# Performance work log

Measured on AMD Instinct MI355X. Metric: run time of the kernel, lower is better.

Reference implementation:

```python
import jax, jax.numpy as jnp
from jax import lax
import numpy as np

EPS = 1e-5


def conv2d(x, w, b, stride, pad):
    y = lax.conv_general_dilated(x, w, (stride, stride), [(pad, pad), (pad, pad)],
                                 dimension_numbers=('NCHW', 'OIHW', 'NCHW'))
    return y + b[None, :, None, None]


def conv_transpose2d(x, w, b, stride, pad, opad):
    # w in torch ConvTranspose2d layout: (Cin, Cout, kH, kW)
    k = w.shape[2]
    w_f = jnp.flip(w, (2, 3)).transpose(1, 0, 2, 3)  # -> OIHW
    lo = k - 1 - pad
    y = lax.conv_general_dilated(x, w_f, (1, 1), [(lo, lo + opad), (lo, lo + opad)],
                                 lhs_dilation=(stride, stride),
                                 dimension_numbers=('NCHW', 'OIHW', 'NCHW'))
    return y + b[None, :, None, None]


def batchnorm(x, g, b):
    # training-mode BN: batch statistics over (N, H, W)
    mean = jnp.mean(x, axis=(0, 2, 3), keepdims=True)
    var = jnp.var(x, axis=(0, 2, 3), keepdims=True)
    return (x - mean) * lax.rsqrt(var + EPS) * g[None, :, None, None] + b[None, :, None, None]


def quantize(z, codebook):
    # z: (B, C, H, W), codebook: (K, C)
    B, C, H, W = z.shape
    zf = z.transpose(0, 2, 3, 1).reshape(-1, C)  # (B*H*W, C)
    # squared Euclidean distances (argmin-equivalent to torch.cdist p=2)
    d2 = (jnp.sum(zf * zf, axis=1, keepdims=True)
          - 2.0 * zf @ codebook.T
          + jnp.sum(codebook * codebook, axis=1)[None, :])
    idx = jnp.argmin(d2, axis=-1)                # (B*H*W,)
    quant = codebook[idx]                        # gather
    loss_embed = jnp.mean((lax.stop_gradient(zf) - quant) ** 2)
    loss_commit = jnp.mean((zf - lax.stop_gradient(quant)) ** 2)
    quant_out = zf + lax.stop_gradient(quant - zf)  # straight-through
    quant_out = quant_out.reshape(B, H, W, C).transpose(0, 3, 1, 2)
    return quant_out, loss_embed, loss_commit, idx.reshape(B, H * W)


def setup_inputs() -> dict:
    key = jax.random.key(0)
    ks = jax.random.split(key, 20)
    f32 = jnp.float32

    def w(k, shape):
        fan_in = int(np.prod(shape[1:]))
        return jax.random.normal(k, shape, f32) / np.sqrt(fan_in)

    B, IMG = 64, 128
    C0, C1, C2, LAT, K = 3, 128, 256, 64, 512
    return {
        'x': jax.random.normal(ks[0], (B, C0, IMG, IMG), f32),
        'enc1_w': w(ks[1], (C1, C0, 3, 3)), 'enc1_b': jnp.zeros((C1,), f32),
        'bn1_g': jnp.ones((C1,), f32), 'bn1_b': jnp.zeros((C1,), f32),
        'enc2_w': w(ks[2], (C2, C1, 3, 3)), 'enc2_b': jnp.zeros((C2,), f32),
        'pre_w': w(ks[3], (LAT, C2, 1, 1)), 'pre_b': jnp.zeros((LAT,), f32),
        'codebook': jax.random.normal(ks[4], (K, LAT), f32),
        'post_w': w(ks[5], (C2, LAT, 1, 1)), 'post_b': jnp.zeros((C2,), f32),
        'dec1_w': w(ks[6], (C2, C1, 3, 3)), 'dec1_b': jnp.zeros((C1,), f32),
        'dbn1_g': jnp.ones((C1,), f32), 'dbn1_b': jnp.zeros((C1,), f32),
        'dec2_w': w(ks[7], (C1, C0, 3, 3)), 'dec2_b': jnp.zeros((C0,), f32),
    }


def reference(x, enc1_w, enc1_b, bn1_g, bn1_b, enc2_w, enc2_b, pre_w, pre_b,
              codebook, post_w, post_b, dec1_w, dec1_b, dbn1_g, dbn1_b,
              dec2_w, dec2_b):
    # encoder
    h = jax.nn.relu(batchnorm(conv2d(x, enc1_w, enc1_b, 2, 1), bn1_g, bn1_b))
    h = conv2d(h, enc2_w, enc2_b, 2, 1)          # (B, 256, 32, 32), no BN/act on last enc conv
    z = conv2d(h, pre_w, pre_b, 1, 0)            # (B, 64, 32, 32)
    # VQ codebook lookup
    q, loss_embed, loss_commit, idx = quantize(z, codebook)
    # decoder
    d = conv2d(q, post_w, post_b, 1, 0)          # (B, 256, 32, 32)
    d = jax.nn.relu(batchnorm(conv_transpose2d(d, dec1_w, dec1_b, 2, 1, 1), dbn1_g, dbn1_b))
    recon = jnp.tanh(conv_transpose2d(d, dec2_w, dec2_b, 2, 1, 1))  # (B, 3, 128, 128)
    return recon, loss_embed, loss_commit, idx
```

## Files before the change

### kernel.cpp

```cpp
#include <hip/hip_runtime.h>

#define EPS 1e-5f

typedef __attribute__((ext_vector_type(8))) short short8;
typedef __attribute__((ext_vector_type(4))) float f32x4;
typedef _Float16 half8v __attribute__((ext_vector_type(8)));

__device__ inline ushort f2bf(float f) {
    uint u = __float_as_uint(f);
    u += 0x7FFFu + ((u >> 16) & 1u);
    return (ushort)(u >> 16);
}
__device__ inline float bf2f(ushort h) { return __uint_as_float(((uint)h) << 16); }
__device__ inline ushort hbits(_Float16 h) { return __builtin_bit_cast(ushort, h); }

#define WS_BN1SUM   0
#define WS_LOSS     512
#define WS_BN1SC    1024
#define WS_BN1SH    1152
#define WS_BN2SC    1280
#define WS_BN2SH    1408
#define WS_CC       1536
#define WS_IDX      2048
#define WS_WT3      67584
#define WS_WT1      83968
#define WS_WT2      378880
#define WS_F        673792
#define WS_BN2S8    804864
#define WS_BN1S8    806912
#define WS_WTE1     808960
#define WS_A        1048576
#define WS_B        34603008
#define WS_Z        WS_A

#define OUT_LOSS_E  3145728
#define OUT_LOSS_C  3145729
#define OUT_IDX     3145730

__global__ __launch_bounds__(256) void k_wt(const float* __restrict__ dec1_w,
                                            const float* __restrict__ enc2_w,
                                            const float* __restrict__ pre_w,
                                            const float* __restrict__ enc1_w,
                                            float* __restrict__ ws) {
    int g = blockIdx.x * 256 + threadIdx.x;
    if (g < 294912) {
        int ci = g & 255, co = (g >> 8) & 127, tap = g >> 15;
        float v = dec1_w[ci * 1152 + co * 9 + tap];
        ushort hi = f2bf(v);
        ushort lo = f2bf(v - bf2f(hi));
        ushort* u16 = (ushort*)(ws + WS_WT1);
        u16[g] = hi;
        u16[294912 + g] = lo;
    } else if (g < 2 * 294912) {
        int h = g - 294912;
        int ci = h & 127, rest = h >> 7;
        int co = rest & 255, tap = rest >> 8;
        float v = enc2_w[co * 1152 + ci * 9 + tap];
        _Float16 hi = (_Float16)v;
        _Float16 lo = (_Float16)((v - (float)hi) * 2048.0f);
        ushort* u16 = (ushort*)(ws + WS_WT2);
        u16[h] = hbits(hi);
        u16[294912 + h] = hbits(lo);
    } else if (g < 2 * 294912 + 16384) {
        int h = g - 2 * 294912;
        int co = h & 63, ci = h >> 6;
        ws[WS_WT3 + h] = pre_w[co * 256 + ci];
    } else if (g < 2 * 294912 + 16384 + 4096) {
        int h = g - (2 * 294912 + 16384);
        int k = h & 31, co = h >> 5;
        float v = (k < 27) ? enc1_w[co * 27 + k] : 0.f;
        _Float16 hi = (_Float16)v;
        _Float16 lo = (_Float16)((v - (float)hi) * 2048.0f);
        ushort* u16 = (ushort*)(ws + WS_WTE1);
        u16[h] = hbits(hi);
        u16[4096 + h] = hbits(lo);
    }
}

__global__ __launch_bounds__(256) void k_F(const float* __restrict__ codebook,
                                           const float* __restrict__ post_w,
                                           const float* __restrict__ post_b,
                                           float* __restrict__ ws) {
    __shared__ __align__(16) float cbr[64];
    int k = blockIdx.x, co = threadIdx.x;
    if (co < 64) cbr[co] = codebook[k * 64 + co];
    __syncthreads();
    float acc = post_b[co];
#pragma unroll
    for (int i = 0; i < 64; i += 4) {
        float4 w4 = *(const float4*)&post_w[co * 64 + i];
        acc = fmaf(cbr[i], w4.x, acc);
        acc = fmaf(cbr[i + 1], w4.y, acc);
        acc = fmaf(cbr[i + 2], w4.z, acc);
        acc = fmaf(cbr[i + 3], w4.w, acc);
    }
    ws[WS_F + k * 256 + co] = acc;
    if (co == 0) {
        float s = 0.f;
        for (int i = 0; i < 64; i++) s += cbr[i] * cbr[i];
        ws[WS_CC + k] = s;
    }
}

__global__ __launch_bounds__(256, 2) void k_enc1(const float* __restrict__ x,
                                                 const float* __restrict__ bias,
                                                 float* __restrict__ ws) {
    __shared__ __align__(16) float raw_s[1950];
    __shared__ __align__(16) ushort As_h[5120], As_l[5120];
    int b = blockIdx.x;
    int n = b >> 5, oy0 = (b & 31) * 2;
    int tid = threadIdx.x, lane = tid & 63, wid = tid >> 6;
    int wy = wid >> 1, wx = wid & 1;
    int l15 = lane & 15, quad = lane >> 4;
    int co0 = wx * 64;
    const ushort* we1h = (const ushort*)(ws + WS_WTE1);
    const ushort* we1l = we1h + 4096;

    half8v Bh[4], Bl[4];
#pragma unroll
    for (int nt = 0; nt < 4; nt++) {
        int src = (co0 + nt * 16 + l15) * 32 + quad * 8;
        Bh[nt] = *(const half8v*)&we1h[src];
        Bl[nt] = *(const half8v*)&we1l[src];
    }

    for (int i = tid; i < 1950; i += 256) {
        int c = i % 130, rest = i / 130;
        int rr = rest % 5, ci = rest / 5;
        int iy = 2 * oy0 - 1 + rr, ix = c - 1;
        float v = 0.f;
        if ((unsigned)iy < 128u && (unsigned)ix < 128u)
            v = x[(n * 3 + ci) * 16384 + iy * 128 + ix];
        raw_s[i] = v;
    }
    __syncthreads();

    for (int i = tid; i < 4096; i += 256) {
        int m = i >> 5, k = i & 31;
        float v = 0.f;
        if (k < 27) {
            int ci = k / 9, t9 = k - ci * 9;
            int ky = t9 / 3, kx = t9 - ky * 3;
            int r = m >> 6, xx = m & 63;
            v = raw_s[(ci * 5 + 2 * r + ky) * 130 + 2 * xx + kx];
        }
        _Float16 hi = (_Float16)v;
        _Float16 lo = (_Float16)((v - (float)hi) * 2048.f);
        As_h[m * 40 + k] = hbits(hi);
        As_l[m * 40 + k] = hbits(lo);
    }
    __syncthreads();

    f32x4 acc1[4][4], acc2[4][4];
#pragma unroll
    for (int nt = 0; nt < 4; nt++) {
        float bv = bias[co0 + nt * 16 + l15];
#pragma unroll
        for (int mt = 0; mt < 4; mt++) {
            acc1[mt][nt] = (f32x4){bv, bv, bv, bv};
            acc2[mt][nt] = (f32x4){0.f, 0.f, 0.f, 0.f};
        }
    }

    half8v Ah[4], Al[4];
#pragma unroll
    for (int mt = 0; mt < 4; mt++) {
        int aoff = (wy * 64 + mt * 16 + l15) * 40 + quad * 8;
        Ah[mt] = *(const half8v*)&As_h[aoff];
        Al[mt] = *(const half8v*)&As_l[aoff];
    }
#pragma unroll
    for (int nt = 0; nt < 4; nt++)
#pragma unroll
        for (int mt = 0; mt < 4; mt++) {
            acc2[mt][nt] = __builtin_amdgcn_mfma_f32_16x16x32_f16(Ah[mt], Bl[nt], acc2[mt][nt], 0, 0, 0);
            acc2[mt][nt] = __builtin_amdgcn_mfma_f32_16x16x32_f16(Al[mt], Bh[nt], acc2[mt][nt], 0, 0, 0);
            acc1[mt][nt] = __builtin_amdgcn_mfma_f32_16x16x32_f16(Ah[mt], Bh[nt], acc1[mt][nt], 0, 0, 0);
        }

    float* h1 = ws + WS_A;
    const float ls = 1.f / 2048.f;
    int oy = oy0 + wy;
#pragma unroll
    for (int mt = 0; mt < 4; mt++) {
        int x0 = mt * 16 + quad * 4;
#pragma unroll
        for (int nt = 0; nt < 4; nt++) {
            int co = co0 + nt * 16 + l15;
            *(float4*)&h1[((n * 128 + co) * 64 + oy) * 64 + x0] =
                make_float4(fmaf(acc2[mt][nt][0], ls, acc1[mt][nt][0]),
                            fmaf(acc2[mt][nt][1], ls, acc1[mt][nt][1]),
                            fmaf(acc2[mt][nt][2], ls, acc1[mt][nt][2]),
                            fmaf(acc2[mt][nt][3], ls, acc1[mt][nt][3]));
        }
    }
    int shadow = (b & 7) * 256;
#pragma unroll
    for (int nt = 0; nt < 4; nt++) {
        float s1 = 0.f, s2 = 0.f;
#pragma unroll
        for (int mt = 0; mt < 4; mt++)
#pragma unroll
            for (int r = 0; r < 4; r++) {
                float v = fmaf(acc2[mt][nt][r], ls, acc1[mt][nt][r]);
                s1 += v; s2 += v * v;
            }
        s1 += __shfl_xor(s1, 16); s1 += __shfl_xor(s1, 32);
        s2 += __shfl_xor(s2, 16); s2 += __shfl_xor(s2, 32);
        if (quad == 0) {
            int co = co0 + nt * 16 + l15;
            atomicAdd(&ws[WS_BN1S8 + shadow + co], s1);
            atomicAdd(&ws[WS_BN1S8 + shadow + 128 + co], s2);
        }
    }
}

__global__ __launch_bounds__(128) void k_bnfin8(const float* __restrict__ sums8,
                                                const float* __restrict__ g,
                                                const float* __restrict__ b,
                                                float* __restrict__ scale,
                                                float* __restrict__ shift) {
    int c = threadIdx.x;
    float s1 = 0.f, s2 = 0.f;
    for (int k = 0; k < 8; k++) {
        s1 += sums8[k * 256 + c];
        s2 += sums8[k * 256 + 128 + c];
    }
    float mean = s1 * (1.f / 262144.f);
    float var = s2 * (1.f / 262144.f) - mean * mean;
    float sc = g[c] * rsqrtf(var + EPS);
    scale[c] = sc;
    shift[c] = b[c] - mean * sc;
}

__global__ __launch_bounds__(256, 2) void k_enc2(const float* __restrict__ bias,
                                                 float* __restrict__ ws) {
    __shared__ __align__(16) uint As_h[6500], As_l[6500];
    __shared__ float scs[128], shs[128];
    int b = blockIdx.x;
    int n = b >> 4, y0 = (b & 15) * 2;
    int tid = threadIdx.x, lane = tid & 63, wid = tid >> 6;
    int l15 = lane & 15, quad = lane >> 4;
    int co0 = wid * 64;
    const float* h1 = ws + WS_A;
    const ushort* w2h = (const ushort*)(ws + WS_WT2);
    const ushort* w2l = w2h + 294912;

    if (tid < 128) { scs[tid] = ws[WS_BN1SC + tid]; shs[tid] = ws[WS_BN1SH + tid]; }

    int Abase[4];
#pragma unroll
    for (int mt = 0; mt < 4; mt++) {
        int m = mt * 16 + l15;
        Abase[mt] = (2 * (m >> 5)) * 2600 + (2 * (m & 31)) * 40 + quad * 8;
    }

    f32x4 acc1[4][4], acc2[4][4];
#pragma unroll
    for (int nt = 0; nt < 4; nt++) {
        float bv = bias[co0 + nt * 16 + l15];
#pragma unroll
        for (int mt = 0; mt < 4; mt++) {
            acc1[mt][nt] = (f32x4){bv, bv, bv, bv};
            acc2[mt][nt] = (f32x4){0.f, 0.f, 0.f, 0.f};
        }
    }

    for (int c0 = 0; c0 < 128; c0 += 32) {
        __syncthreads();
        if (tid < 80) {
            int p = tid & 15, row = tid >> 4;
            As_h[row * 1300 + p] = 0;
            As_l[row * 1300 + p] = 0;
        }
        for (int i = tid; i < 1280; i += 256) {
            int p = i & 15, g = i >> 4;
            int row = g >> 4, colg = g & 15;
            int in_y = 2 * y0 - 1 + row;
            int ci0 = c0 + 2 * p;
            float av[4] = {0.f, 0.f, 0.f, 0.f}, bv[4] = {0.f, 0.f, 0.f, 0.f};
            if ((unsigned)in_y < 64u) {
                const float* bp = h1 + (n * 128 + ci0) * 4096 + in_y * 64 + colg * 4;
                float4 va = *(const float4*)bp;
                float4 vb = *(const float4*)(bp + 4096);
                float sa = scs[ci0], ta = shs[ci0];
                float sb = scs[ci0 + 1], tb = shs[ci0 + 1];
                av[0] = fmaxf(fmaf(va.x, sa, ta), 0.f); av[1] = fmaxf(fmaf(va.y, sa, ta), 0.f);
                av[2] = fmaxf(fmaf(va.z, sa, ta), 0.f); av[3] = fmaxf(fmaf(va.w, sa, ta), 0.f);
                bv[0] = fmaxf(fmaf(vb.x, sb, tb), 0.f); bv[1] = fmaxf(fmaf(vb.y, sb, tb), 0.f);
                bv[2] = fmaxf(fmaf(vb.z, sb, tb), 0.f); bv[3] = fmaxf(fmaf(vb.w, sb, tb), 0.f);
            }
            int wbase = row * 1300 + (colg * 4 + 1) * 20 + p;
#pragma unroll
            for (int j = 0; j < 4; j++) {
                _Float16 ah = (_Float16)av[j], bh = (_Float16)bv[j];
                _Float16 al = (_Float16)((av[j] - (float)ah) * 2048.f);
                _Float16 bl = (_Float16)((bv[j] - (float)bh) * 2048.f);
                As_h[wbase + j * 20] = (uint)hbits(ah) | ((uint)hbits(bh) << 16);
                As_l[wbase + j * 20] = (uint)hbits(al) | ((uint)hbits(bl) << 16);
            }
        }
        __syncthreads();
        const ushort* ah16 = (const ushort*)As_h;
        const ushort* al16 = (const ushort*)As_l;
#pragma unroll
        for (int tap = 0; tap < 9; tap++) {
            int ky = tap / 3, kx = tap - ky * 3;
            int toff = ky * 2600 + kx * 40;
            half8v Bh[4], Bl[4];
#pragma unroll
            for (int nt = 0; nt < 4; nt++) {
                int src = (tap * 256 + co0 + nt * 16 + l15) * 128 + c0 + quad * 8;
                Bh[nt] = *(const half8v*)&w2h[src];
                Bl[nt] = *(const half8v*)&w2l[src];
            }
            half8v Ah[4], Al[4];
#pragma unroll
            for (int mt = 0; mt < 4; mt++) {
                Ah[mt] = *(const half8v*)&ah16[Abase[mt] + toff];
                Al[mt] = *(const half8v*)&al16[Abase[mt] + toff];
            }
#pragma unroll
            for (int nt = 0; nt < 4; nt++)
#pragma unroll
                for (int mt = 0; mt < 4; mt++) {
                    acc2[mt][nt] = __builtin_amdgcn_mfma_f32_16x16x32_f16(Ah[mt], Bl[nt], acc2[mt][nt], 0, 0, 0);
                    acc2[mt][nt] = __builtin_amdgcn_mfma_f32_16x16x32_f16(Al[mt], Bh[nt], acc2[mt][nt], 0, 0, 0);
                    acc1[mt][nt] = __builtin_amdgcn_mfma_f32_16x16x32_f16(Ah[mt], Bh[nt], acc1[mt][nt], 0, 0, 0);
                }
        }
    }

    float* h2 = ws + WS_B;
    const float ls = 1.f / 2048.f;
#pragma unroll
    for (int mt = 0; mt < 4; mt++) {
        int mloc = mt * 16 + quad * 4;
        int y = y0 + (mloc >> 5), x = mloc & 31;
#pragma unroll
        for (int nt = 0; nt < 4; nt++) {
            int co = co0 + nt * 16 + l15;
            *(float4*)&h2[(n * 256 + co) * 1024 + y * 32 + x] =
                make_float4(fmaf(acc2[mt][nt][0], ls, acc1[mt][nt][0]),
                            fmaf(acc2[mt][nt][1], ls, acc1[mt][nt][1]),
                            fmaf(acc2[mt][nt][2], ls, acc1[mt][nt][2]),
                            fmaf(acc2[mt][nt][3], ls, acc1[mt][nt][3]));
        }
    }
}

__global__ __launch_bounds__(256) void k_pre(const float* __restrict__ bias,
                                             float* __restrict__ ws) {
    __shared__ __align__(16) float a_s[8 * 128];
    __shared__ __align__(16) float b_s[8 * 64];
    int p0 = blockIdx.x * 128;
    int n = p0 >> 10, sp0 = p0 & 1023;
    int tid = threadIdx.x;
    int px4 = tid & 31, cg = tid >> 5;
    int co8 = cg * 8;
    const float* h2 = ws + WS_B;
    const float* wt3 = ws + WS_WT3;

    float acc[4][8];
#pragma unroll
    for (int r = 0; r < 4; r++)
#pragma unroll
        for (int j = 0; j < 8; j++) acc[r][j] = bias[co8 + j];

    for (int c0 = 0; c0 < 256; c0 += 8) {
        __syncthreads();
#pragma unroll
        for (int it = 0; it < 4; it++) {
            int t = tid + it * 256;
            a_s[t] = h2[n * 262144 + (c0 + (t >> 7)) * 1024 + sp0 + (t & 127)];
        }
#pragma unroll
        for (int it = 0; it < 2; it++) {
            int t = tid + it * 256;
            b_s[t] = wt3[(c0 + (t >> 6)) * 64 + (t & 63)];
        }
        __syncthreads();
#pragma unroll
        for (int ci = 0; ci < 8; ci++) {
            float4 av = *(const float4*)&a_s[ci * 128 + px4 * 4];
            float4 w0 = *(const float4*)&b_s[ci * 64 + co8];
            float4 w1 = *(const float4*)&b_s[ci * 64 + co8 + 4];
            float wv[8] = {w0.x, w0.y, w0.z, w0.w, w1.x, w1.y, w1.z, w1.w};
            float a[4] = {av.x, av.y, av.z, av.w};
#pragma unroll
            for (int j = 0; j < 8; j++)
#pragma unroll
                for (int r = 0; r < 4; r++) acc[r][j] = fmaf(a[r], wv[j], acc[r][j]);
        }
    }
    float* z = ws + WS_Z;
#pragma unroll
    for (int r = 0; r < 4; r++) {
        int p = p0 + px4 * 4 + r;
        *(float4*)&z[p * 64 + co8] = make_float4(acc[r][0], acc[r][1], acc[r][2], acc[r][3]);
        *(float4*)&z[p * 64 + co8 + 4] = make_float4(acc[r][4], acc[r][5], acc[r][6], acc[r][7]);
    }
}

__global__ __launch_bounds__(256, 2) void k_vq(const float* __restrict__ codebook,
                                               float* __restrict__ out,
                                               float* __restrict__ ws) {
    __shared__ __align__(16) float cb_s[128 * 64];
    __shared__ __align__(16) float cc_s[128];
    int tid = threadIdx.x;
    int p = blockIdx.x * 256 + tid;
    const float* z = ws + WS_Z + p * 64;
    float4 z4[16];
#pragma unroll
    for (int i = 0; i < 16; i++) z4[i] = *(const float4*)&z[i * 4];
    float zz = 0.f;
#pragma unroll
    for (int i = 0; i < 16; i++)
        zz += z4[i].x * z4[i].x + z4[i].y * z4[i].y + z4[i].z * z4[i].z + z4[i].w * z4[i].w;

    float best = 3.4e38f;
    int bidx = 0;
    for (int k0 = 0; k0 < 512; k0 += 128) {
        __syncthreads();
#pragma unroll
        for (int it = 0; it < 32; it++) {
            int t = tid + it * 256;
            cb_s[t] = codebook[k0 * 64 + t];
        }
        if (tid < 128) cc_s[tid] = ws[WS_CC + k0 + tid];
        __syncthreads();
        for (int k = 0; k < 128; k++) {
            const float4* cp = (const float4*)&cb_s[k * 64];
            float d0 = 0.f, d1 = 0.f, d2 = 0.f, d3 = 0.f;
#pragma unroll
            for (int i = 0; i < 16; i += 4) {
                float4 c0v = cp[i], c1v = cp[i + 1], c2v = cp[i + 2], c3v = cp[i + 3];
                d0 += z4[i].x * c0v.x + z4[i].y * c0v.y + z4[i].z * c0v.z + z4[i].w * c0v.w;
                d1 += z4[i + 1].x * c1v.x + z4[i + 1].y * c1v.y + z4[i + 1].z * c1v.z + z4[i + 1].w * c1v.w;
                d2 += z4[i + 2].x * c2v.x + z4[i + 2].y * c2v.y + z4[i + 2].z * c2v.z + z4[i + 2].w * c2v.w;
                d3 += z4[i + 3].x * c3v.x + z4[i + 3].y * c3v.y + z4[i + 3].z * c3v.z + z4[i + 3].w * c3v.w;
            }
            float dot = (d0 + d1) + (d2 + d3);
            float d = fmaf(-2.f, dot, zz) + cc_s[k];
            if (d < best) { best = d; bidx = k0 + k; }
        }
    }
    out[OUT_IDX + p] = (float)bidx;
    ((int*)(ws + WS_IDX))[p] = bidx;

    float e = 0.f;
    const float4* q = (const float4*)&codebook[bidx * 64];
#pragma unroll
    for (int i = 0; i < 16; i++) {
        float4 qq = q[i];
        float d0 = z4[i].x - qq.x, d1 = z4[i].y - qq.y;
        float d2 = z4[i].z - qq.z, d3 = z4[i].w - qq.w;
        e += d0 * d0 + d1 * d1 + d2 * d2 + d3 * d3;
    }
#pragma unroll
    for (int off = 32; off; off >>= 1) e += __shfl_down(e, off);
    if ((tid & 63) == 0) atomicAdd(&ws[WS_LOSS], e);
}

__global__ void k_loss(float* __restrict__ out, const float* __restrict__ ws) {
    if (threadIdx.x == 0) {
        float v = ws[WS_LOSS] * (1.f / (65536.f * 64.f));
        out[OUT_LOSS_E] = v;
        out[OUT_LOSS_C] = v;
    }
}

__global__ __launch_bounds__(256) void k_gather(float* __restrict__ ws) {
    int tid = threadIdx.x;
    const int* idx = (const int*)(ws + WS_IDX);
    const float* F = ws + WS_F;
    float* dpx = ws + WS_B;
    int base = blockIdx.x * 64;
    for (int i = 0; i < 64; i++) {
        int row = idx[base + i];
        dpx[(base + i) * 256 + tid] = F[row * 256 + tid];
    }
}

__global__ __launch_bounds__(256, 2) void k_dec1(const float* __restrict__ bias,
                                                 float* __restrict__ ws) {
    __shared__ __align__(16) short As_h[5280], As_l[5280];
    __shared__ __align__(16) short Bs_h[4096], Bs_l[4096];
    int bx = blockIdx.x;
    int tile = bx & 511, phase = bx >> 9;
    int py = phase >> 1, px = phase & 1;
    int n_img = tile >> 3, a0 = (tile & 7) * 4;
    int tid = threadIdx.x, lane = tid & 63, wid = tid >> 6;
    int wy = wid >> 1, wx = wid & 1;
    int l15 = lane & 15, quad = lane >> 4;

    int ntY = py + 1, ntX = px + 1, ntap = ntY * ntX;
    int tap_off[4], tap_w[4];
    {
        int ti = 0;
        for (int ty = 0; ty < ntY; ty++)
            for (int tx = 0; tx < ntX; tx++) {
                int dy = py ? 1 - ty : 0, ky = py ? 2 * ty : 1;
                int dx = px ? 1 - tx : 0, kx = px ? 2 * tx : 1;
                tap_off[ti] = (dy * 33 + dx) * 32;
                tap_w[ti] = ky * 3 + kx;
                ti++;
            }
    }

    int Aoff[4];
#pragma unroll
    for (int mt = 0; mt < 4; mt++) {
        int m_loc = wy * 64 + mt * 16 + l15;
        Aoff[mt] = ((m_loc >> 5) * 33 + (m_loc & 31)) * 32 + quad * 8;
    }
    int Boff[4];
#pragma unroll
    for (int nt = 0; nt < 4; nt++)
        Boff[nt] = (wx * 64 + nt * 16 + l15) * 32 + quad * 8;

    f32x4 acc[4][4];
#pragma unroll
    for (int nt = 0; nt < 4; nt++) {
        float bv = bias[wx * 64 + nt * 16 + l15];
#pragma unroll
        for (int mt = 0; mt < 4; mt++) acc[mt][nt] = (f32x4){bv, bv, bv, bv};
    }

    const float* dpx = ws + WS_B;
    const ushort* wbh = (const ushort*)(ws + WS_WT1);
    const ushort* wbl = wbh + 294912;

    for (int c0 = 0; c0 < 256; c0 += 32) {
        __syncthreads();
        for (int i = tid; i < 1320; i += 256) {
            int p5 = i >> 3, q = i & 7;
            int rr = p5 / 33, cc = p5 - rr * 33;
            int a_in = a0 + rr;
            float4 v = make_float4(0.f, 0.f, 0.f, 0.f);
            if (a_in < 32 && cc < 32)
                v = *(const float4*)&dpx[(n_img * 1024 + a_in * 32 + cc) * 256 + c0 + q * 4];
            ushort h0 = f2bf(v.x), h1 = f2bf(v.y), h2 = f2bf(v.z), h3v = f2bf(v.w);
            ushort l0 = f2bf(v.x - bf2f(h0)), l1 = f2bf(v.y - bf2f(h1));
            ushort l2 = f2bf(v.z - bf2f(h2)), l3 = f2bf(v.w - bf2f(h3v));
            int d = p5 * 32 + q * 4;
            *(uint*)&As_h[d]     = (uint)h0 | ((uint)h1 << 16);
            *(uint*)&As_h[d + 2] = (uint)h2 | ((uint)h3v << 16);
            *(uint*)&As_l[d]     = (uint)l0 | ((uint)l1 << 16);
            *(uint*)&As_l[d + 2] = (uint)l2 | ((uint)l3 << 16);
        }
        for (int t = 0; t < ntap; t++) {
            if (t) __syncthreads();
            int tw = tap_w[t];
            for (int i = tid; i < 512; i += 256) {
                int co = i >> 2, q = i & 3;
                int src = (tw * 128 + co) * 256 + c0 + q * 8;
                *(uint4*)&Bs_h[co * 32 + q * 8] = *(const uint4*)&wbh[src];
                *(uint4*)&Bs_l[co * 32 + q * 8] = *(const uint4*)&wbl[src];
            }
            __syncthreads();
            int ao = tap_off[t];
            short8 Ah[4], Al[4];
#pragma unroll
            for (int mt = 0; mt < 4; mt++) {
                Ah[mt] = *(const short8*)&As_h[Aoff[mt] + ao];
                Al[mt] = *(const short8*)&As_l[Aoff[mt] + ao];
            }
#pragma unroll
            for (int nt = 0; nt < 4; nt++) {
                short8 Bh = *(const short8*)&Bs_h[Boff[nt]];
                short8 Bl = *(const short8*)&Bs_l[Boff[nt]];
#pragma unroll
                for (int mt = 0; mt < 4; mt++) {
                    acc[mt][nt] = __builtin_amdgcn_mfma_f32_16x16x32_bf16(Ah[mt], Bh, acc[mt][nt], 0, 0, 0);
                    acc[mt][nt] = __builtin_amdgcn_mfma_f32_16x16x32_bf16(Ah[mt], Bl, acc[mt][nt], 0, 0, 0);
                    acc[mt][nt] = __builtin_amdgcn_mfma_f32_16x16x32_bf16(Al[mt], Bh, acc[mt][nt], 0, 0, 0);
                }
            }
        }
    }

    float* h3n = ws + WS_A;
#pragma unroll
    for (int mt = 0; mt < 4; mt++) {
#pragma unroll
        for (int r = 0; r < 4; r++) {
            int m_glob = tile * 128 + wy * 64 + mt * 16 + quad * 4 + r;
            int a = (m_glob >> 5) & 31, bb = m_glob & 31;
            int y = 2 * a + py, x = 2 * bb + px;
            float* rowp = &h3n[(((m_glob >> 10) * 64 + y) * 64 + x) * 128 + wx * 64];
#pragma unroll
            for (int nt = 0; nt < 4; nt++) rowp[nt * 16 + l15] = acc[mt][nt][r];
        }
    }
    int shadow = (bx & 7) * 256;
#pragma unroll
    for (int nt = 0; nt < 4; nt++) {
        float s1 = 0.f, s2 = 0.f;
#pragma unroll
        for (int mt = 0; mt < 4; mt++)
#pragma unroll
            for (int r = 0; r < 4; r++) {
                float v = acc[mt][nt][r];
                s1 += v; s2 += v * v;
            }
        s1 += __shfl_xor(s1, 16); s1 += __shfl_xor(s1, 32);
        s2 += __shfl_xor(s2, 16); s2 += __shfl_xor(s2, 32);
        if (quad == 0) {
            int co = wx * 64 + nt * 16 + l15;
            atomicAdd(&ws[WS_BN2S8 + shadow + co], s1);
            atomicAdd(&ws[WS_BN2S8 + shadow + 128 + co], s2);
        }
    }
}

__global__ __launch_bounds__(1024, 2) void k_dec2(const float* __restrict__ w,
                                                  const float* __restrict__ bias,
                                                  float* __restrict__ out,
                                                  float* __restrict__ ws) {
    __shared__ __align__(16) float in_s[8 * 5 * 66];
    __shared__ __align__(16) float w_s[8 * 9 * 3];
    __shared__ float scs[128], shs[128];
    int n = blockIdx.y;
    int atile = blockIdx.x;
    int a0 = atile * 4;
    int tid = threadIdx.x;
    int phase = tid >> 8;
    int py = phase >> 1, px = phase & 1;
    int tidl = tid & 255;
    int b = tidl & 63, r4 = tidl >> 6;
    int ntsh = py + px;
    int ntap = 1 << ntsh;
    const float* h3n = ws + WS_A;

    if (tid < 128) { scs[tid] = ws[WS_BN2SC + tid]; shs[tid] = ws[WS_BN2SH + tid]; }

    float acc[3] = {bias[0], bias[1], bias[2]};
    for (int c0 = 0; c0 < 128; c0 += 8) {
        __syncthreads();
        if (tid < 660) {
            int ciq = tid & 1, s = tid >> 1;
            int cL = s % 66, row = s / 66;
            int iy = a0 + row;
            float r0 = 0.f, r1 = 0.f, r2 = 0.f, r3 = 0.f;
            if (iy < 64 && cL < 64) {
                float4 v = *(const float4*)&h3n[((n * 64 + iy) * 64 + cL) * 128 + c0 + ciq * 4];
                int cb = c0 + ciq * 4;
                r0 = fmaxf(fmaf(v.x, scs[cb], shs[cb]), 0.f);
                r1 = fmaxf(fmaf(v.y, scs[cb + 1], shs[cb + 1]), 0.f);
                r2 = fmaxf(fmaf(v.z, scs[cb + 2], shs[cb + 2]), 0.f);
                r3 = fmaxf(fmaf(v.w, scs[cb + 3], shs[cb + 3]), 0.f);
            }
            int ci0 = ciq * 4;
            in_s[(ci0 + 0) * 330 + row * 66 + cL] = r0;
            in_s[(ci0 + 1) * 330 + row * 66 + cL] = r1;
            in_s[(ci0 + 2) * 330 + row * 66 + cL] = r2;
            in_s[(ci0 + 3) * 330 + row * 66 + cL] = r3;
        }
        if (tid < 8 * 9 * 3) {
            int co = tid % 3, q = tid / 3;
            int ci = q / 9, tap = q - ci * 9;
            w_s[q * 3 + co] = w[(c0 + ci) * 27 + co * 9 + tap];
        }
        __syncthreads();
#pragma unroll
        for (int ci = 0; ci < 8; ci++) {
#pragma unroll
            for (int tt = 0; tt < 4; tt++) {
                if (tt >= ntap) break;
                int ty = tt >> px, tx = tt & px;
                int ky = py ? 2 * ty : 1;
                int kx = px ? 2 * tx : 1;
                int dyv = py ? 1 - ty : 0;
                int dxv = px ? 1 - tx : 0;
                float v = in_s[ci * 330 + (r4 + dyv) * 66 + b + dxv];
                const float* wp = &w_s[(ci * 9 + ky * 3 + kx) * 3];
                acc[0] = fmaf(v, wp[0], acc[0]);
                acc[1] = fmaf(v, wp[1], acc[1]);
                acc[2] = fmaf(v, wp[2], acc[2]);
            }
        }
    }
    int y = 2 * (a0 + r4) + py, xcol = 2 * b + px;
#pragma unroll
    for (int co = 0; co < 3; co++)
        out[(n * 3 + co) * 16384 + y * 128 + xcol] = tanhf(acc[co]);
}

extern "C" void kernel_launch(void* const* d_in, const int* in_sizes, int n_in,
                              void* d_out, int out_size, void* d_ws, size_t ws_size,
                              hipStream_t stream) {
    const float* x       = (const float*)d_in[0];
    const float* enc1_w  = (const float*)d_in[1];
    const float* enc1_b  = (const float*)d_in[2];
    const float* bn1_g   = (const float*)d_in[3];
    const float* bn1_b   = (const float*)d_in[4];
    const float* enc2_w  = (const float*)d_in[5];
    const float* enc2_b  = (const float*)d_in[6];
    const float* pre_w   = (const float*)d_in[7];
    const float* pre_b   = (const float*)d_in[8];
    const float* codebook= (const float*)d_in[9];
    const float* post_w  = (const float*)d_in[10];
    const float* post_b  = (const float*)d_in[11];
    const float* dec1_w  = (const float*)d_in[12];
    const float* dec1_b  = (const float*)d_in[13];
    const float* dbn1_g  = (const float*)d_in[14];
    const float* dbn1_b  = (const float*)d_in[15];
    const float* dec2_w  = (const float*)d_in[16];
    const float* dec2_b  = (const float*)d_in[17];
    float* out = (float*)d_out;
    float* ws  = (float*)d_ws;

    hipMemsetAsync(ws, 0, 4096, stream);
    hipMemsetAsync(ws + WS_BN2S8, 0, 2 * 8 * 256 * 4, stream);

    k_wt<<<2384, 256, 0, stream>>>(dec1_w, enc2_w, pre_w, enc1_w, ws);
    k_F<<<512, 256, 0, stream>>>(codebook, post_w, post_b, ws);
    k_enc1<<<2048, 256, 0, stream>>>(x, enc1_b, ws);
    k_bnfin8<<<1, 128, 0, stream>>>(ws + WS_BN1S8, bn1_g, bn1_b,
                                    ws + WS_BN1SC, ws + WS_BN1SH);
    k_enc2<<<1024, 256, 0, stream>>>(enc2_b, ws);
    k_pre<<<512, 256, 0, stream>>>(pre_b, ws);
    k_vq<<<256, 256, 0, stream>>>(codebook, out, ws);
    k_loss<<<1, 64, 0, stream>>>(out, ws);
    k_gather<<<1024, 256, 0, stream>>>(ws);
    k_dec1<<<2048, 256, 0, stream>>>(dec1_b, ws);
    k_bnfin8<<<1, 128, 0, stream>>>(ws + WS_BN2S8, dbn1_g, dbn1_b,
                                    ws + WS_BN2SC, ws + WS_BN2SH);
    k_dec2<<<dim3(16, 64), 1024, 0, stream>>>(dec2_w, dec2_b, out, ws);
}
```

Baseline: 856.7 us.

## Compute VQ distances with split-fp16 MFMA and derive loss from min distance

The scalar FP32 codebook-distance loop in k_vq becomes split-fp16 (hi/lo) MFMA matrix multiplies. Each block handles 64 pixels and each wave scans 128 codes, then an argmin is reduced across lanes and waves with ties broken toward the lower index. The codebook is pre-split into fp16 hi/lo in k_wt. The loss is now taken as zz plus the minimum distance rather than recomputed against the gathered code. This can cause small rounding differences and argmin flips on near-ties, and the loss can pick up cancellation error.

```diff
diff --git a/kernel.cpp b/kernel.cpp
--- a/kernel.cpp
+++ b/kernel.cpp
@@ -14,7 +14,6 @@
 __device__ inline float bf2f(ushort h) { return __uint_as_float(((uint)h) << 16); }
 __device__ inline ushort hbits(_Float16 h) { return __builtin_bit_cast(ushort, h); }
 
-#define WS_BN1SUM   0
 #define WS_LOSS     512
 #define WS_BN1SC    1024
 #define WS_BN1SH    1152
@@ -29,6 +28,7 @@
 #define WS_BN2S8    804864
 #define WS_BN1S8    806912
 #define WS_WTE1     808960
+#define WS_CBS      819200
 #define WS_A        1048576
 #define WS_B        34603008
 #define WS_Z        WS_A
@@ -41,6 +41,7 @@
                                             const float* __restrict__ enc2_w,
                                             const float* __restrict__ pre_w,
                                             const float* __restrict__ enc1_w,
+                                            const float* __restrict__ codebook,
                                             float* __restrict__ ws) {
     int g = blockIdx.x * 256 + threadIdx.x;
     if (g < 294912) {
@@ -74,6 +75,14 @@
         ushort* u16 = (ushort*)(ws + WS_WTE1);
         u16[h] = hbits(hi);
         u16[4096 + h] = hbits(lo);
+    } else if (g < 2 * 294912 + 16384 + 4096 + 32768) {
+        int h = g - (2 * 294912 + 16384 + 4096);
+        float v = codebook[h];
+        _Float16 hi = (_Float16)v;
+        _Float16 lo = (_Float16)((v - (float)hi) * 2048.0f);
+        ushort* u16 = (ushort*)(ws + WS_CBS);
+        u16[h] = hbits(hi);
+        u16[32768 + h] = hbits(lo);
     }
 }
 
@@ -402,64 +411,137 @@
     }
 }
 
-__global__ __launch_bounds__(256, 2) void k_vq(const float* __restrict__ codebook,
-                                               float* __restrict__ out,
+__global__ __launch_bounds__(256, 2) void k_vq(float* __restrict__ out,
                                                float* __restrict__ ws) {
-    __shared__ __align__(16) float cb_s[128 * 64];
-    __shared__ __align__(16) float cc_s[128];
-    int tid = threadIdx.x;
-    int p = blockIdx.x * 256 + tid;
-    const float* z = ws + WS_Z + p * 64;
-    float4 z4[16];
-#pragma unroll
-    for (int i = 0; i < 16; i++) z4[i] = *(const float4*)&z[i * 4];
-    float zz = 0.f;
-#pragma unroll
-    for (int i = 0; i < 16; i++)
-        zz += z4[i].x * z4[i].x + z4[i].y * z4[i].y + z4[i].z * z4[i].z + z4[i].w * z4[i].w;
-
-    float best = 3.4e38f;
-    int bidx = 0;
-    for (int k0 = 0; k0 < 512; k0 += 128) {
-        __syncthreads();
-#pragma unroll
-        for (int it = 0; it < 32; it++) {
-            int t = tid + it * 256;
-            cb_s[t] = codebook[k0 * 64 + t];
-        }
-        if (tid < 128) cc_s[tid] = ws[WS_CC + k0 + tid];
-        __syncthreads();
-        for (int k = 0; k < 128; k++) {
-            const float4* cp = (const float4*)&cb_s[k * 64];
-            float d0 = 0.f, d1 = 0.f, d2 = 0.f, d3 = 0.f;
-#pragma unroll
-            for (int i = 0; i < 16; i += 4) {
-                float4 c0v = cp[i], c1v = cp[i + 1], c2v = cp[i + 2], c3v = cp[i + 3];
-                d0 += z4[i].x * c0v.x + z4[i].y * c0v.y + z4[i].z * c0v.z + z4[i].w * c0v.w;
-                d1 += z4[i + 1].x * c1v.x + z4[i + 1].y * c1v.y + z4[i + 1].z * c1v.z + z4[i + 1].w * c1v.w;
-                d2 += z4[i + 2].x * c2v.x + z4[i + 2].y * c2v.y + z4[i + 2].z * c2v.z + z4[i + 2].w * c2v.w;
-                d3 += z4[i + 3].x * c3v.x + z4[i + 3].y * c3v.y + z4[i + 3].z * c3v.z + z4[i + 3].w * c3v.w;
-            }
-            float dot = (d0 + d1) + (d2 + d3);
-            float d = fmaf(-2.f, dot, zz) + cc_s[k];
-            if (d < best) { best = d; bidx = k0 + k; }
-        }
-    }
-    out[OUT_IDX + p] = (float)bidx;
-    ((int*)(ws + WS_IDX))[p] = bidx;
-
-    float e = 0.f;
-    const float4* q = (const float4*)&codebook[bidx * 64];
-#pragma unroll
-    for (int i = 0; i < 16; i++) {
-        float4 qq = q[i];
-        float d0 = z4[i].x - qq.x, d1 = z4[i].y - qq.y;
-        float d2 = z4[i].z - qq.z, d3 = z4[i].w - qq.w;
-        e += d0 * d0 + d1 * d1 + d2 * d2 + d3 * d3;
-    }
-#pragma unroll
-    for (int off = 32; off; off >>= 1) e += __shfl_down(e, off);
-    if ((tid & 63) == 0) atomicAdd(&ws[WS_LOSS], e);
+    __shared__ __align__(16) ushort Ash[64 * 72], Asl[64 * 72];
+    __shared__ float zz_s[64];
+    __shared__ float red_s[256];
+    __shared__ int red_i[256];
+    int p0 = blockIdx.x * 64;
+    int tid = threadIdx.x, lane = tid & 63, wid = tid >> 6;
+    int l15 = lane & 15, quad = lane >> 4;
+    const float* z = ws + WS_Z;
+    const ushort* cbh = (const ushort*)(ws + WS_CBS);
+    const ushort* cbl = cbh + 32768;
+
+    for (int i = tid; i < 1024; i += 256) {
+        int m = i >> 4, k4 = (i & 15) * 4;
+        float4 v = *(const float4*)&z[(p0 + m) * 64 + k4];
+        _Float16 h0 = (_Float16)v.x, h1 = (_Float16)v.y, h2 = (_Float16)v.z, h3 = (_Float16)v.w;
+        _Float16 l0 = (_Float16)((v.x - (float)h0) * 2048.f);
+        _Float16 l1 = (_Float16)((v.y - (float)h1) * 2048.f);
+        _Float16 l2 = (_Float16)((v.z - (float)h2) * 2048.f);
+        _Float16 l3 = (_Float16)((v.w - (float)h3) * 2048.f);
+        int d = m * 72 + k4;
+        *(uint*)&Ash[d]     = (uint)hbits(h0) | ((uint)hbits(h1) << 16);
+        *(uint*)&Ash[d + 2] = (uint)hbits(h2) | ((uint)hbits(h3) << 16);
+        *(uint*)&Asl[d]     = (uint)hbits(l0) | ((uint)hbits(l1) << 16);
+        *(uint*)&Asl[d + 2] = (uint)hbits(l2) | ((uint)hbits(l3) << 16);
+    }
+    if (tid < 64) {
+        const float* zp = &z[(p0 + tid) * 64];
+        float s = 0.f;
+#pragma unroll
+        for (int k = 0; k < 64; k += 4) {
+            float4 v = *(const float4*)&zp[k];
+            s += v.x * v.x + v.y * v.y + v.z * v.z + v.w * v.w;
+        }
+        zz_s[tid] = s;
+    }
+    __syncthreads();
+
+    float best_s[4][4];
+    int best_i[4][4];
+#pragma unroll
+    for (int mt = 0; mt < 4; mt++)
+#pragma unroll
+        for (int r = 0; r < 4; r++) { best_s[mt][r] = 3.4e38f; best_i[mt][r] = 0; }
+
+    const float ls = 1.f / 2048.f;
+    for (int pass = 0; pass < 2; pass++) {
+        f32x4 acc1[4][4], acc2[4][4];
+#pragma unroll
+        for (int mt = 0; mt < 4; mt++)
+#pragma unroll
+            for (int nt = 0; nt < 4; nt++) {
+                acc1[mt][nt] = (f32x4){0.f, 0.f, 0.f, 0.f};
+                acc2[mt][nt] = (f32x4){0.f, 0.f, 0.f, 0.f};
+            }
+#pragma unroll
+        for (int kc = 0; kc < 2; kc++) {
+            half8v Ah[4], Al[4];
+#pragma unroll
+            for (int mt = 0; mt < 4; mt++) {
+                int aoff = (mt * 16 + l15) * 72 + kc * 32 + quad * 8;
+                Ah[mt] = *(const half8v*)&Ash[aoff];
+                Al[mt] = *(const half8v*)&Asl[aoff];
+            }
+#pragma unroll
+            for (int nt = 0; nt < 4; nt++) {
+                int code = wid * 128 + pass * 64 + nt * 16 + l15;
+                int src = code * 64 + kc * 32 + quad * 8;
+                half8v Bh = *(const half8v*)&cbh[src];
+                half8v Bl = *(const half8v*)&cbl[src];
+#pragma unroll
+                for (int mt = 0; mt < 4; mt++) {
+                    acc2[mt][nt] = __builtin_amdgcn_mfma_f32_16x16x32_f16(Ah[mt], Bl, acc2[mt][nt], 0, 0, 0);
+                    acc2[mt][nt] = __builtin_amdgcn_mfma_f32_16x16x32_f16(Al[mt], Bh, acc2[mt][nt], 0, 0, 0);
+                    acc1[mt][nt] = __builtin_amdgcn_mfma_f32_16x16x32_f16(Ah[mt], Bh, acc1[mt][nt], 0, 0, 0);
+                }
+            }
+        }
+#pragma unroll
+        for (int nt = 0; nt < 4; nt++) {
+            int code = wid * 128 + pass * 64 + nt * 16 + l15;
+            float cc = ws[WS_CC + code];
+#pragma unroll
+            for (int mt = 0; mt < 4; mt++)
+#pragma unroll
+                for (int r = 0; r < 4; r++) {
+                    float dot = fmaf(acc2[mt][nt][r], ls, acc1[mt][nt][r]);
+                    float s = fmaf(-2.f, dot, cc);
+                    if (s < best_s[mt][r] || (s == best_s[mt][r] && code < best_i[mt][r])) {
+                        best_s[mt][r] = s; best_i[mt][r] = code;
+                    }
+                }
+        }
+    }
+
+#pragma unroll
+    for (int mt = 0; mt < 4; mt++)
+#pragma unroll
+        for (int r = 0; r < 4; r++) {
+            float s = best_s[mt][r];
+            int ix = best_i[mt][r];
+#pragma unroll
+            for (int off = 1; off < 16; off <<= 1) {
+                float so = __shfl_xor(s, off);
+                int io = __shfl_xor(ix, off);
+                if (so < s || (so == s && io < ix)) { s = so; ix = io; }
+            }
+            if (l15 == 0) {
+                int px = mt * 16 + quad * 4 + r;
+                red_s[wid * 64 + px] = s;
+                red_i[wid * 64 + px] = ix;
+            }
+        }
+    __syncthreads();
+    if (tid < 64) {
+        float s = red_s[tid];
+        int ix = red_i[tid];
+#pragma unroll
+        for (int w = 1; w < 4; w++) {
+            float so = red_s[w * 64 + tid];
+            int io = red_i[w * 64 + tid];
+            if (so < s || (so == s && io < ix)) { s = so; ix = io; }
+        }
+        out[OUT_IDX + p0 + tid] = (float)ix;
+        ((int*)(ws + WS_IDX))[p0 + tid] = ix;
+        float e = fmaxf(zz_s[tid] + s, 0.f);
+#pragma unroll
+        for (int off = 32; off; off >>= 1) e += __shfl_down(e, off);
+        if (tid == 0) atomicAdd(&ws[WS_LOSS], e);
+    }
 }
 
 __global__ void k_loss(float* __restrict__ out, const float* __restrict__ ws) {
@@ -714,14 +796,14 @@
     hipMemsetAsync(ws, 0, 4096, stream);
     hipMemsetAsync(ws + WS_BN2S8, 0, 2 * 8 * 256 * 4, stream);
 
-    k_wt<<<2384, 256, 0, stream>>>(dec1_w, enc2_w, pre_w, enc1_w, ws);
+    k_wt<<<2512, 256, 0, stream>>>(dec1_w, enc2_w, pre_w, enc1_w, codebook, ws);
     k_F<<<512, 256, 0, stream>>>(codebook, post_w, post_b, ws);
     k_enc1<<<2048, 256, 0, stream>>>(x, enc1_b, ws);
     k_bnfin8<<<1, 128, 0, stream>>>(ws + WS_BN1S8, bn1_g, bn1_b,
                                     ws + WS_BN1SC, ws + WS_BN1SH);
     k_enc2<<<1024, 256, 0, stream>>>(enc2_b, ws);
     k_pre<<<512, 256, 0, stream>>>(pre_b, ws);
-    k_vq<<<256, 256, 0, stream>>>(codebook, out, ws);
+    k_vq<<<1024, 256, 0, stream>>>(out, ws);
     k_loss<<<1, 64, 0, stream>>>(out, ws);
     k_gather<<<1024, 256, 0, stream>>>(ws);
     k_dec1<<<2048, 256, 0, stream>>>(dec1_b, ws);
```

Measured after the change: 695.9 us. 1.23x faster.
